# Kernel optimization log

Measured on AMD Instinct MI355X. Metric: run time of the kernel, lower is better.

Reference implementation:

```python
import jax, jax.numpy as jnp
import numpy as np

N_VERBS = 500
N_ROLES = 190
VOCAB = 2000
R = 6            # max_role_count
EMB = 512        # embed_hidden == lstm_hidden
MLP = 1024       # mlp_hidden
C = 512          # conv base size
H = W = 7
NP = H * W
NC = C + 2       # conv channels + 2 coord channels


def _lin(k, fan_in, fan_out):
    kw, kb = jax.random.split(k)
    s = 1.0 / np.sqrt(fan_in)
    return (jax.random.uniform(kw, (fan_in, fan_out), jnp.float32, -s, s),
            jax.random.uniform(kb, (fan_out,), jnp.float32, -s, s))


def setup_inputs() -> dict:
    key = jax.random.key(0)
    ks = jax.random.split(key, 16)
    inp = {}
    inp['conv_feat'] = jax.random.normal(ks[0], (2, C, H, W), jnp.float32)
    inp['verbs'] = jax.random.randint(ks[1], (2,), 0, N_VERBS, jnp.int32)
    inp['roles'] = jax.random.randint(ks[2], (2, R), 0, N_ROLES, jnp.int32)
    inp['verb_emb'] = jax.random.normal(ks[3], (N_VERBS, EMB), jnp.float32)
    inp['role_emb'] = jax.random.normal(ks[4], (N_ROLES + 1, EMB), jnp.float32)
    inp['vW1'], inp['vb1'] = _lin(ks[5], NP * C, MLP)
    inp['vW2'], inp['vb2'] = _lin(ks[6], MLP, MLP)
    inp['vW3'], inp['vb3'] = _lin(ks[7], MLP, N_VERBS)
    inp['gW1'], inp['gb1'] = _lin(ks[8], 2 * NC + EMB, MLP)
    inp['gW2'], inp['gb2'] = _lin(ks[9], MLP, MLP)
    inp['gW3'], inp['gb3'] = _lin(ks[10], MLP, 2 * MLP)
    inp['gW4'], inp['gb4'] = _lin(ks[11], 2 * MLP, 4 * MLP)
    inp['fW1'], inp['fb1'] = _lin(ks[12], 4 * MLP, 4 * MLP)
    inp['fW2'], inp['fb2'] = _lin(ks[13], 4 * MLP, 2 * MLP)
    inp['fW3'], inp['fb3'] = _lin(ks[14], 2 * MLP, VOCAB)
    return inp


def _coords():
    c = jnp.linspace(-4.0, 4.0, H)
    x = jnp.broadcast_to(c[None, :], (H, W))   # x varies along width
    y = jnp.broadcast_to(c[:, None], (H, W))   # y varies along height
    return jnp.stack([x, y]).reshape(2, NP).T  # [NP, 2]


def reference(conv_feat, verbs, roles, verb_emb, role_emb,
              vW1, vb1, vW2, vb2, vW3, vb3,
              gW1, gb1, gW2, gb2, gW3, gb3, gW4, gb4,
              fW1, fb1, fW2, fb2, fW3, fb3):
    relu = jax.nn.relu
    B = conv_feat.shape[0]

    # verb head
    flat = conv_feat.reshape(B, NP * C)
    v = relu(flat @ vW1 + vb1)
    v = relu(v @ vW2 + vb2)
    verb_pred = v @ vW3 + vb3                                  # [B, N_VERBS]

    # role-verb query
    rv = (verb_emb[verbs][:, None, :] * role_emb[roles]).reshape(B * R, EMB)

    # per-role conv features + coord channels -> [Bu, NP, NC]
    feat = jnp.broadcast_to(conv_feat[:, None], (B, R, C, H, W)).reshape(B * R, C, NP)
    feat = jnp.concatenate([feat.transpose(0, 2, 1),
                            jnp.broadcast_to(_coords()[None], (B * R, NP, 2))], axis=2)

    # first g layer: concat([o_j, o_i, qst]) @ gW1 == split matmuls + broadcast add
    Wa, Wb, Wc = gW1[:NC], gW1[NC:2 * NC], gW1[2 * NC:]
    A = feat @ Wa          # pairs with conv1 (index j)
    Bm = feat @ Wb         # pairs with conv2 (index i)
    Q = rv @ Wc
    h = relu(A[:, None, :, :] + Bm[:, :, None, :] + Q[:, None, None, :] + gb1)  # [Bu, NP, NP, MLP]
    h = relu(h @ gW2 + gb2)
    h = relu(h @ gW3 + gb3)
    h = relu(h @ gW4 + gb4)                                    # [Bu, NP, NP, 4*MLP]
    g = h.sum(axis=(1, 2))                                     # [Bu, 4*MLP]

    f = relu(g @ fW1 + fb1)
    f = relu(f @ fW2 + fb2)
    f = f @ fW3 + fb3                                          # [Bu, VOCAB]
    role_predict = f.reshape(B, R, VOCAB)
    return verb_pred, role_predict
```

## Files before the change

### kernel.cpp

```cpp
#include <hip/hip_runtime.h>
#include <cstdint>

typedef _Float16 f16;
typedef f16 f16x8 __attribute__((ext_vector_type(8)));
typedef f16 f16x4 __attribute__((ext_vector_type(4)));
typedef float f32x4 __attribute__((ext_vector_type(4)));

#define GROUP_ROWS 2560
#define VALID_ROWS 2401
#define TPG 10
#define NGROUP 12

template <bool B> struct BoolC { static constexpr bool value = B; };

__device__ __forceinline__ void gll16(const void* g, void* l) {
  __builtin_amdgcn_global_load_lds((const __attribute__((address_space(1))) void*)g,
                                   (__attribute__((address_space(3))) void*)l, 16, 0, 0);
}

__global__ void wtrans_all(const float* __restrict__ gW2, const float* __restrict__ gW3,
                           const float* __restrict__ gW4, f16* __restrict__ W2t,
                           f16* __restrict__ W3t, f16* __restrict__ W4t) {
  __shared__ float t[32][33];
  int blk = blockIdx.x;
  const float* W; f16* Wt; int K, N, local;
  if (blk < 1024)      { W = gW2; Wt = W2t; K = 1024; N = 1024; local = blk; }
  else if (blk < 3072) { W = gW3; Wt = W3t; K = 1024; N = 2048; local = blk - 1024; }
  else                 { W = gW4; Wt = W4t; K = 2048; N = 4096; local = blk - 3072; }
  int ntn = N >> 5;
  int k0 = (local / ntn) * 32, n0 = (local % ntn) * 32;
  int tx = threadIdx.x & 31, ty = threadIdx.x >> 5;
#pragma unroll
  for (int j = 0; j < 4; ++j)
    t[ty + j * 8][tx] = W[(size_t)(k0 + ty + j * 8) * N + n0 + tx];
  __syncthreads();
#pragma unroll
  for (int j = 0; j < 4; ++j)
    Wt[(size_t)(n0 + ty + j * 8) * K + k0 + tx] = (f16)t[tx][ty + j * 8];
}

__global__ void build_rv(const float* __restrict__ verb_emb, const float* __restrict__ role_emb,
                         const int* __restrict__ verbs, const int* __restrict__ roles,
                         float* __restrict__ rv) {
  int g = blockIdx.x;
  int b = g / 6;
  int v = verbs[b], ro = roles[g];
  for (int e = threadIdx.x; e < 512; e += 256)
    rv[g * 512 + e] = verb_emb[(size_t)v * 512 + e] * role_emb[(size_t)ro * 512 + e];
}

__global__ void build_AB(const float* __restrict__ conv, const float* __restrict__ gW1,
                         float* __restrict__ A, float* __restrict__ Bm) {
  int blk = blockIdx.x;
  int nq = blk & 3, bp = blk >> 2;
  int p = bp % 49, b = bp / 49;
  int n = nq * 256 + threadIdx.x;
  float accA = 0.f, accB = 0.f;
  for (int k = 0; k < 514; ++k) {
    float s;
    if (k < 512) s = conv[((size_t)b * 512 + k) * 49 + p];
    else {
      int c7 = (k == 512) ? (p % 7) : (p / 7);
      s = (float)(c7 - 3) * (4.0f / 3.0f);
    }
    accA = fmaf(s, gW1[(size_t)k * 1024 + n], accA);
    accB = fmaf(s, gW1[(size_t)(514 + k) * 1024 + n], accB);
  }
  size_t row = ((size_t)b * 49 + p) * 1024;
  A[row + n] = accA;
  Bm[row + n] = accB;
}

__global__ void build_h1(const float* __restrict__ A, const float* __restrict__ Bm,
                         const float* __restrict__ Q, const float* __restrict__ gb1,
                         f16* __restrict__ h1, int g0) {
  int rc = blockIdx.x;
  int gl = rc / GROUP_ROWS;
  int li = rc % GROUP_ROWS;
  int g = g0 + gl;
  int b = g / 6;
  int kk = threadIdx.x * 4;
  f16x4* dst = (f16x4*)(h1 + (size_t)rc * 1024 + kk);
  if (li >= VALID_ROWS) {
    f16x4 z = {(f16)0.f, (f16)0.f, (f16)0.f, (f16)0.f};
    *dst = z;
    return;
  }
  int i = li / 49, j = li % 49;
  const float4 a = *(const float4*)(A + ((size_t)b * 49 + j) * 1024 + kk);
  const float4 bb = *(const float4*)(Bm + ((size_t)b * 49 + i) * 1024 + kk);
  const float4 q = *(const float4*)(Q + (size_t)g * 1024 + kk);
  const float4 bi = *(const float4*)(gb1 + kk);
  float v0 = a.x + bb.x + q.x + bi.x;
  float v1 = a.y + bb.y + q.y + bi.y;
  float v2 = a.z + bb.z + q.z + bi.z;
  float v3 = a.w + bb.w + q.w + bi.w;
  f16x4 r;
  r.x = (f16)(v0 > 0.f ? v0 : 0.f);
  r.y = (f16)(v1 > 0.f ? v1 : 0.f);
  r.z = (f16)(v2 > 0.f ? v2 : 0.f);
  r.w = (f16)(v3 > 0.f ? v3 : 0.f);
  *dst = r;
}

#define WV4 asm volatile("s_waitcnt vmcnt(4)" ::: "memory")
#define WV0 asm volatile("s_waitcnt vmcnt(0)" ::: "memory")

#define LDSA(buf, mf, cc) (*(const f16x8*)(ldsc + (buf)*32768 + arow + (mf)*2048 + (cc)*16))
#define LDSB(buf, nf, cc) (*(const f16x8*)(ldsc + 65536 + (buf)*32768 + brow + (nf)*2048 + (cc)*16))

#define LOADB(BF, buf) { \
  BF[0][0] = LDSB(buf, 0, c0); BF[0][1] = LDSB(buf, 0, c1); \
  BF[1][0] = LDSB(buf, 1, c0); BF[1][1] = LDSB(buf, 1, c1); \
  BF[2][0] = LDSB(buf, 2, c0); BF[2][1] = LDSB(buf, 2, c1); \
  BF[3][0] = LDSB(buf, 3, c0); BF[3][1] = LDSB(buf, 3, c1); }

#define STAGE_A(t, h) { \
  const f16* _g = Aglo + (long)(h) * (128L * K) + (long)(t) * 64; \
  char* _l = ldsc + ((t)&1)*32768 + ((h)*128 + wave*16)*128; \
  gll16(_g, _l); gll16(_g + 8L*K, _l + 1024); }

#define STAGE_B(t, h) { \
  const f16* _g = Bglo + (long)(h) * (128L * K) + (long)(t) * 64; \
  char* _l = ldsc + 65536 + ((t)&1)*32768 + ((h)*128 + wave*16)*128; \
  gll16(_g, _l); gll16(_g + 8L*K, _l + 1024); }

#define PHASE(q, buf, BF, STG, WT, POST) { \
  f16x8 a00 = LDSA(buf, 2*(q), c0);   f16x8 a01 = LDSA(buf, 2*(q), c1); \
  f16x8 a10 = LDSA(buf, 2*(q)+1, c0); f16x8 a11 = LDSA(buf, 2*(q)+1, c1); \
  STG; \
  WT; \
  __builtin_amdgcn_s_barrier(); \
  __builtin_amdgcn_s_setprio(1); \
  _Pragma("unroll") \
  for (int nf = 0; nf < 4; ++nf) { \
    acc[2*(q)][nf]   = __builtin_amdgcn_mfma_f32_16x16x32_f16(a00, BF[nf][0], acc[2*(q)][nf], 0, 0, 0); \
    acc[2*(q)][nf]   = __builtin_amdgcn_mfma_f32_16x16x32_f16(a01, BF[nf][1], acc[2*(q)][nf], 0, 0, 0); \
    acc[2*(q)+1][nf] = __builtin_amdgcn_mfma_f32_16x16x32_f16(a10, BF[nf][0], acc[2*(q)+1][nf], 0, 0, 0); \
    acc[2*(q)+1][nf] = __builtin_amdgcn_mfma_f32_16x16x32_f16(a11, BF[nf][1], acc[2*(q)+1][nf], 0, 0, 0); \
  } \
  __builtin_amdgcn_s_setprio(0); \
  POST; \
  __builtin_amdgcn_s_barrier(); \
}

template <int FUSED>
__global__ __launch_bounds__(512, 2)
void gemm256(const f16* __restrict__ A, const f16* __restrict__ Bt,
             const float* __restrict__ bias, f16* __restrict__ C,
             float* __restrict__ P, int N, int K, int ntiles, int mtile_off) {
  __shared__ __align__(16) char ldsbuf[131072];
  char* ldsc = ldsbuf;
  const int tid = threadIdx.x;
  const int wave = tid >> 6, lane = tid & 63;
  const int wm = wave >> 2, wn = wave & 3;
  const int lr = lane & 15, lk = lane >> 4;
  const int c0 = lk ^ (lr & 7), c1 = c0 ^ 4;
  const int arow = (wm * 128 + lr) * 128;
  const int brow = (wn * 64 + lr) * 128;

  int nwg = gridDim.x, id = blockIdx.x;
  int qq = nwg >> 3, rr8 = nwg & 7;
  int xcd = id & 7, idx = id >> 3;
  int wg = (xcd < rr8 ? xcd * (qq + 1) : rr8 * (qq + 1) + (xcd - rr8) * qq) + idx;
  const int mtile = wg / ntiles, ntile = wg % ntiles;
  const long m0 = (long)mtile * 256, n0 = (long)ntile * 256;

  const int srow = lane >> 3;
  const int schunk = (lane & 7) ^ srow;
  const f16* Aglo = A + (m0 + wave * 16 + srow) * (long)K + schunk * 8;
  const f16* Bglo = Bt + (n0 + wave * 16 + srow) * (long)K + schunk * 8;

  f32x4 acc[8][4] = {};
  f16x8 bFa[4][2], bFb[4][2];

  const int NI = K >> 7;

  STAGE_B(0, 0); STAGE_B(0, 1);
  STAGE_A(0, 0); STAGE_A(0, 1);
  STAGE_B(1, 0); STAGE_B(1, 1);
  WV4;
  __builtin_amdgcn_s_barrier();
  LOADB(bFa, 0);

  auto run_iter = [&](int i, auto lastTag) {
    constexpr bool LAST = decltype(lastTag)::value;
    PHASE(0, 0, bFa, STAGE_A(2*i+1, 0), ;, ;);
    PHASE(1, 0, bFa, STAGE_A(2*i+1, 1), ;, ;);
    PHASE(2, 0, bFa, if constexpr (!LAST) STAGE_B(2*i+2, 0), ;, ;);
    PHASE(3, 0, bFa, if constexpr (!LAST) STAGE_B(2*i+2, 1),
                 if constexpr (LAST) { WV0; } else { WV4; },
                 LOADB(bFb, 1));
    PHASE(0, 1, bFb, if constexpr (!LAST) STAGE_A(2*i+2, 0), ;, ;);
    PHASE(1, 1, bFb, if constexpr (!LAST) STAGE_A(2*i+2, 1), ;, ;);
    PHASE(2, 1, bFb, if constexpr (!LAST) STAGE_B(2*i+3, 0), ;, ;);
    PHASE(3, 1, bFb, if constexpr (!LAST) STAGE_B(2*i+3, 1),
                 if constexpr (!LAST) { WV4; },
                 if constexpr (!LAST) LOADB(bFa, 0));
  };
#pragma unroll 1
  for (int i = 0; i < NI - 1; ++i) run_iter(i, BoolC<false>{});
  run_iter(NI - 1, BoolC<true>{});

  if (FUSED == 0) {
#pragma unroll
    for (int mf = 0; mf < 8; ++mf) {
      const long row = m0 + wm * 128 + mf * 16 + lk * 4;
#pragma unroll
      for (int nf = 0; nf < 4; ++nf) {
        const long col = n0 + wn * 64 + nf * 16 + lr;
        const float bv = bias[col];
#pragma unroll
        for (int r = 0; r < 4; ++r) {
          float v = acc[mf][nf][r] + bv;
          v = v > 0.f ? v : 0.f;
          C[(row + r) * N + col] = (f16)v;
        }
      }
    }
  } else {
    float* csum = (float*)ldsc;
    const int mrel = (mtile % TPG) * 256 + wm * 128;
#pragma unroll
    for (int nf = 0; nf < 4; ++nf) {
      const int col = (int)n0 + wn * 64 + nf * 16 + lr;
      const float bv = bias[col];
      float s = 0.f;
#pragma unroll
      for (int mf = 0; mf < 8; ++mf) {
        const int rb = mrel + mf * 16 + lk * 4;
#pragma unroll
        for (int r = 0; r < 4; ++r) {
          float v = acc[mf][nf][r] + bv;
          v = v > 0.f ? v : 0.f;
          if (rb + r < VALID_ROWS) s += v;
        }
      }
      s += __shfl_xor(s, 16);
      s += __shfl_xor(s, 32);
      if (lk == 0) csum[wm * 256 + wn * 64 + nf * 16 + lr] = s;
    }
    __syncthreads();
    for (int t = tid; t < 256; t += 512)
      P[(long)(mtile_off + mtile) * N + n0 + t] = csum[t] + csum[256 + t];
  }
}

__global__ void reduce_g(const float* __restrict__ P, float* __restrict__ g) {
  int idx = blockIdx.x * 256 + threadIdx.x;
  if (idx >= NGROUP * 4096) return;
  int gi = idx >> 12, n = idx & 4095;
  float s = 0.f;
#pragma unroll
  for (int t = 0; t < TPG; ++t) s += P[(size_t)(gi * TPG + t) * 4096 + n];
  g[idx] = s;
}

template <int M>
__global__ void skinny_part(const float* __restrict__ X, const float* __restrict__ W,
                            float* __restrict__ P, int K, int N, int kchunk) {
  int n = blockIdx.x * 256 + threadIdx.x;
  int k0 = blockIdx.y * kchunk;
  int k1 = k0 + kchunk;
  if (k1 > K) k1 = K;
  if (n >= N) return;
  float acc[M];
#pragma unroll
  for (int m = 0; m < M; ++m) acc[m] = 0.f;
  for (int k = k0; k < k1; ++k) {
    float w = W[(size_t)k * N + n];
#pragma unroll
    for (int m = 0; m < M; ++m) acc[m] = fmaf(X[(size_t)m * K + k], w, acc[m]);
  }
#pragma unroll
  for (int m = 0; m < M; ++m) P[((size_t)blockIdx.y * M + m) * N + n] = acc[m];
}

template <int RELU>
__global__ void skinny_fin(const float* __restrict__ P, const float* __restrict__ bias,
                           float* __restrict__ dst, int M, int N, int KC) {
  int idx = blockIdx.x * 256 + threadIdx.x;
  if (idx >= M * N) return;
  int m = idx / N, n = idx - m * N;
  float s = bias ? bias[n] : 0.f;
  for (int kc = 0; kc < KC; ++kc) s += P[((size_t)kc * M + m) * N + n];
  if (RELU) s = s > 0.f ? s : 0.f;
  dst[idx] = s;
}

static inline void skinny(const float* X, const float* W, const float* bias, float* dst,
                          float* sp, int Mrows, int K, int N, int relu, hipStream_t stream) {
  int KC = K >> 4;
  if (KC > 64) KC = 64;
  if (KC < 1) KC = 1;
  int kchunk = (K + KC - 1) / KC;
  dim3 g1((N + 255) / 256, KC);
  if (Mrows == 2)
    skinny_part<2><<<g1, 256, 0, stream>>>(X, W, sp, K, N, kchunk);
  else
    skinny_part<12><<<g1, 256, 0, stream>>>(X, W, sp, K, N, kchunk);
  int blocks = (Mrows * N + 255) / 256;
  if (relu)
    skinny_fin<1><<<blocks, 256, 0, stream>>>(sp, bias, dst, Mrows, N, KC);
  else
    skinny_fin<0><<<blocks, 256, 0, stream>>>(sp, bias, dst, Mrows, N, KC);
}

extern "C" void kernel_launch(void* const* d_in, const int* in_sizes, int n_in,
                              void* d_out, int out_size, void* d_ws, size_t ws_size,
                              hipStream_t stream) {
  const float* conv = (const float*)d_in[0];
  const int* verbs = (const int*)d_in[1];
  const int* roles = (const int*)d_in[2];
  const float* verb_emb = (const float*)d_in[3];
  const float* role_emb = (const float*)d_in[4];
  const float* vW1 = (const float*)d_in[5];
  const float* vb1 = (const float*)d_in[6];
  const float* vW2 = (const float*)d_in[7];
  const float* vb2 = (const float*)d_in[8];
  const float* vW3 = (const float*)d_in[9];
  const float* vb3 = (const float*)d_in[10];
  const float* gW1 = (const float*)d_in[11];
  const float* gb1 = (const float*)d_in[12];
  const float* gW2 = (const float*)d_in[13];
  const float* gb2 = (const float*)d_in[14];
  const float* gW3 = (const float*)d_in[15];
  const float* gb3 = (const float*)d_in[16];
  const float* gW4 = (const float*)d_in[17];
  const float* gb4 = (const float*)d_in[18];
  const float* fW1 = (const float*)d_in[19];
  const float* fb1 = (const float*)d_in[20];
  const float* fW2 = (const float*)d_in[21];
  const float* fb2 = (const float*)d_in[22];
  const float* fW3 = (const float*)d_in[23];
  const float* fb3 = (const float*)d_in[24];
  float* out = (float*)d_out;

  char* w = (char*)d_ws;
  auto alloc = [&](size_t bytes) {
    char* p = w;
    w += (bytes + 255) & ~(size_t)255;
    return p;
  };
  f16* W2t = (f16*)alloc((size_t)1024 * 1024 * 2);
  f16* W3t = (f16*)alloc((size_t)2048 * 1024 * 2);
  f16* W4t = (f16*)alloc((size_t)4096 * 2048 * 2);
  float* P4 = (float*)alloc((size_t)NGROUP * TPG * 4096 * 4);
  float* Abuf = (float*)alloc((size_t)2 * 49 * 1024 * 4);
  float* Bbuf = (float*)alloc((size_t)2 * 49 * 1024 * 4);
  float* Qbuf = (float*)alloc((size_t)12 * 1024 * 4);
  float* rvb = (float*)alloc((size_t)12 * 512 * 4);
  float* gbuf = (float*)alloc((size_t)12 * 4096 * 4);
  float* sp = (float*)alloc((size_t)64 * 12 * 4096 * 4);
  float* f1b = (float*)alloc((size_t)12 * 4096 * 4);
  float* f2b = (float*)alloc((size_t)12 * 2048 * 4);
  float* v1b = (float*)alloc((size_t)2 * 1024 * 4);
  float* v2b = (float*)alloc((size_t)2 * 1024 * 4);

  size_t used = (size_t)(w - (char*)d_ws);
  size_t remain = ws_size > used ? ws_size - used : 0;
  static const int opts[6] = {12, 6, 4, 3, 2, 1};
  int gpc = 1;
  for (int i = 0; i < 6; ++i) {
    size_t need = (size_t)opts[i] * GROUP_ROWS * 4096 * 2 + 4096;
    if (need <= remain) { gpc = opts[i]; break; }
  }
  f16* h1 = (f16*)alloc((size_t)gpc * GROUP_ROWS * 1024 * 2);
  f16* h2 = (f16*)alloc((size_t)gpc * GROUP_ROWS * 1024 * 2);
  f16* h3 = (f16*)alloc((size_t)gpc * GROUP_ROWS * 2048 * 2);
  int nchunks = NGROUP / gpc;

  wtrans_all<<<1024 + 2048 + 8192, 256, 0, stream>>>(gW2, gW3, gW4, W2t, W3t, W4t);

  build_rv<<<12, 256, 0, stream>>>(verb_emb, role_emb, verbs, roles, rvb);
  build_AB<<<98 * 4, 256, 0, stream>>>(conv, gW1, Abuf, Bbuf);
  skinny(rvb, gW1 + (size_t)1028 * 1024, nullptr, Qbuf, sp, 12, 512, 1024, 0, stream);

  skinny(conv, vW1, vb1, v1b, sp, 2, 25088, 1024, 1, stream);
  skinny(v1b, vW2, vb2, v2b, sp, 2, 1024, 1024, 1, stream);
  skinny(v2b, vW3, vb3, out, sp, 2, 1024, 500, 0, stream);

  for (int c = 0; c < nchunks; ++c) {
    int g0 = c * gpc;
    int Mc = gpc * GROUP_ROWS;
    int mt = Mc / 256;
    build_h1<<<Mc, 256, 0, stream>>>(Abuf, Bbuf, Qbuf, gb1, h1, g0);
    gemm256<0><<<4 * mt, 512, 0, stream>>>(h1, W2t, gb2, h2, nullptr, 1024, 1024, 4, 0);
    gemm256<0><<<8 * mt, 512, 0, stream>>>(h2, W3t, gb3, h3, nullptr, 2048, 1024, 8, 0);
    gemm256<1><<<16 * mt, 512, 0, stream>>>(h3, W4t, gb4, nullptr, P4, 4096, 2048, 16, g0 * TPG);
  }
  reduce_g<<<(NGROUP * 4096 + 255) / 256, 256, 0, stream>>>(P4, gbuf);

  skinny(gbuf, fW1, fb1, f1b, sp, 12, 4096, 4096, 1, stream);
  skinny(f1b, fW2, fb2, f2b, sp, 12, 4096, 2048, 1, stream);
  skinny(f2b, fW3, fb3, out + 1000, sp, 12, 2048, 2000, 0, stream);

  (void)in_sizes; (void)n_in; (void)out_size; (void)ws_size;
}
```

Baseline: 1.162 ms.

## Switch GEMM inner loop to 32x32x16 MFMA and stage epilogue through LDS

Replaces the 16x16x32 f16 MFMA tiling with 32x32x16 MFMA instructions, so each wave computes a 128x64 tile as 4x2 blocks of 32x32 with f32x16 accumulators. LDS fragment addressing and the XOR swizzle keys are recomputed for the new lane layout. This needs fewer LDS fragment reads and fewer MFMA issues per unit of work. The non-fused epilogue now writes bias+ReLU results into LDS and then emits coalesced 16-byte row stores, and the fused reduction is adapted to the new register layout. The cost is extra barriers and an LDS round trip in the epilogue.

Result: slower. 1.268 ms (+9.1%).

```diff
diff --git a/kernel.cpp b/kernel.cpp
--- a/kernel.cpp
+++ b/kernel.cpp
@@ -5,6 +5,7 @@
 typedef f16 f16x8 __attribute__((ext_vector_type(8)));
 typedef f16 f16x4 __attribute__((ext_vector_type(4)));
 typedef float f32x4 __attribute__((ext_vector_type(4)));
+typedef float f32x16 __attribute__((ext_vector_type(16)));
 
 #define GROUP_ROWS 2560
 #define VALID_ROWS 2401
@@ -106,14 +107,14 @@
 #define WV4 asm volatile("s_waitcnt vmcnt(4)" ::: "memory")
 #define WV0 asm volatile("s_waitcnt vmcnt(0)" ::: "memory")
 
-#define LDSA(buf, mf, cc) (*(const f16x8*)(ldsc + (buf)*32768 + arow + (mf)*2048 + (cc)*16))
-#define LDSB(buf, nf, cc) (*(const f16x8*)(ldsc + 65536 + (buf)*32768 + brow + (nf)*2048 + (cc)*16))
+#define LDSA(buf, q, CK) (*(const f16x8*)(ldsc + (buf)*32768 + arow + (q)*4096 + (CK)))
+#define LDSB(buf, nb, CK) (*(const f16x8*)(ldsc + 65536 + (buf)*32768 + brow + (nb)*4096 + (CK)))
 
 #define LOADB(BF, buf) { \
-  BF[0][0] = LDSB(buf, 0, c0); BF[0][1] = LDSB(buf, 0, c1); \
-  BF[1][0] = LDSB(buf, 1, c0); BF[1][1] = LDSB(buf, 1, c1); \
-  BF[2][0] = LDSB(buf, 2, c0); BF[2][1] = LDSB(buf, 2, c1); \
-  BF[3][0] = LDSB(buf, 3, c0); BF[3][1] = LDSB(buf, 3, c1); }
+  BF[0][0] = LDSB(buf, 0, ck0); BF[0][1] = LDSB(buf, 0, ck1); \
+  BF[0][2] = LDSB(buf, 0, ck2); BF[0][3] = LDSB(buf, 0, ck3); \
+  BF[1][0] = LDSB(buf, 1, ck0); BF[1][1] = LDSB(buf, 1, ck1); \
+  BF[1][2] = LDSB(buf, 1, ck2); BF[1][3] = LDSB(buf, 1, ck3); }
 
 #define STAGE_A(t, h) { \
   const f16* _g = Aglo + (long)(h) * (128L * K) + (long)(t) * 64; \
@@ -126,19 +127,20 @@
   gll16(_g, _l); gll16(_g + 8L*K, _l + 1024); }
 
 #define PHASE(q, buf, BF, STG, WT, POST) { \
-  f16x8 a00 = LDSA(buf, 2*(q), c0);   f16x8 a01 = LDSA(buf, 2*(q), c1); \
-  f16x8 a10 = LDSA(buf, 2*(q)+1, c0); f16x8 a11 = LDSA(buf, 2*(q)+1, c1); \
+  f16x8 a0 = LDSA(buf, q, ck0); f16x8 a1 = LDSA(buf, q, ck1); \
+  f16x8 a2 = LDSA(buf, q, ck2); f16x8 a3 = LDSA(buf, q, ck3); \
   STG; \
   WT; \
   __builtin_amdgcn_s_barrier(); \
   __builtin_amdgcn_s_setprio(1); \
-  _Pragma("unroll") \
-  for (int nf = 0; nf < 4; ++nf) { \
-    acc[2*(q)][nf]   = __builtin_amdgcn_mfma_f32_16x16x32_f16(a00, BF[nf][0], acc[2*(q)][nf], 0, 0, 0); \
-    acc[2*(q)][nf]   = __builtin_amdgcn_mfma_f32_16x16x32_f16(a01, BF[nf][1], acc[2*(q)][nf], 0, 0, 0); \
-    acc[2*(q)+1][nf] = __builtin_amdgcn_mfma_f32_16x16x32_f16(a10, BF[nf][0], acc[2*(q)+1][nf], 0, 0, 0); \
-    acc[2*(q)+1][nf] = __builtin_amdgcn_mfma_f32_16x16x32_f16(a11, BF[nf][1], acc[2*(q)+1][nf], 0, 0, 0); \
-  } \
+  acc[q][0] = __builtin_amdgcn_mfma_f32_32x32x16_f16(a0, BF[0][0], acc[q][0], 0, 0, 0); \
+  acc[q][1] = __builtin_amdgcn_mfma_f32_32x32x16_f16(a0, BF[1][0], acc[q][1], 0, 0, 0); \
+  acc[q][0] = __builtin_amdgcn_mfma_f32_32x32x16_f16(a1, BF[0][1], acc[q][0], 0, 0, 0); \
+  acc[q][1] = __builtin_amdgcn_mfma_f32_32x32x16_f16(a1, BF[1][1], acc[q][1], 0, 0, 0); \
+  acc[q][0] = __builtin_amdgcn_mfma_f32_32x32x16_f16(a2, BF[0][2], acc[q][0], 0, 0, 0); \
+  acc[q][1] = __builtin_amdgcn_mfma_f32_32x32x16_f16(a2, BF[1][2], acc[q][1], 0, 0, 0); \
+  acc[q][0] = __builtin_amdgcn_mfma_f32_32x32x16_f16(a3, BF[0][3], acc[q][0], 0, 0, 0); \
+  acc[q][1] = __builtin_amdgcn_mfma_f32_32x32x16_f16(a3, BF[1][3], acc[q][1], 0, 0, 0); \
   __builtin_amdgcn_s_setprio(0); \
   POST; \
   __builtin_amdgcn_s_barrier(); \
@@ -154,10 +156,14 @@
   const int tid = threadIdx.x;
   const int wave = tid >> 6, lane = tid & 63;
   const int wm = wave >> 2, wn = wave & 3;
-  const int lr = lane & 15, lk = lane >> 4;
-  const int c0 = lk ^ (lr & 7), c1 = c0 ^ 4;
-  const int arow = (wm * 128 + lr) * 128;
-  const int brow = (wn * 64 + lr) * 128;
+  const int l31 = lane & 31, hi = lane >> 5;
+  const int key = lane & 7;
+  const int ck0 = ((0 + hi) ^ key) * 16;
+  const int ck1 = ((2 + hi) ^ key) * 16;
+  const int ck2 = ((4 + hi) ^ key) * 16;
+  const int ck3 = ((6 + hi) ^ key) * 16;
+  const int arow = (wm * 128 + l31) * 128;
+  const int brow = (wn * 64 + l31) * 128;
 
   int nwg = gridDim.x, id = blockIdx.x;
   int qq = nwg >> 3, rr8 = nwg & 7;
@@ -171,8 +177,8 @@
   const f16* Aglo = A + (m0 + wave * 16 + srow) * (long)K + schunk * 8;
   const f16* Bglo = Bt + (n0 + wave * 16 + srow) * (long)K + schunk * 8;
 
-  f32x4 acc[8][4] = {};
-  f16x8 bFa[4][2], bFb[4][2];
+  f32x16 acc[4][2] = {};
+  f16x8 bFa[2][4], bFb[2][4];
 
   const int NI = K >> 7;
 
@@ -203,42 +209,54 @@
   run_iter(NI - 1, BoolC<true>{});
 
   if (FUSED == 0) {
-#pragma unroll
-    for (int mf = 0; mf < 8; ++mf) {
-      const long row = m0 + wm * 128 + mf * 16 + lk * 4;
-#pragma unroll
-      for (int nf = 0; nf < 4; ++nf) {
-        const long col = n0 + wn * 64 + nf * 16 + lr;
-        const float bv = bias[col];
-#pragma unroll
-        for (int r = 0; r < 4; ++r) {
-          float v = acc[mf][nf][r] + bv;
+    __syncthreads();
+    f16* lt = (f16*)ldsc;
+#pragma unroll
+    for (int q = 0; q < 4; ++q) {
+#pragma unroll
+      for (int nb = 0; nb < 2; ++nb) {
+        const int lcol = wn * 64 + nb * 32 + l31;
+        const float bv = bias[n0 + lcol];
+        const int rb = wm * 128 + q * 32 + 4 * hi;
+#pragma unroll
+        for (int reg = 0; reg < 16; ++reg) {
+          const int row = rb + (reg & 3) + 8 * (reg >> 2);
+          float v = acc[q][nb][reg] + bv;
           v = v > 0.f ? v : 0.f;
-          C[(row + r) * N + col] = (f16)v;
+          lt[row * 256 + lcol] = (f16)v;
         }
       }
     }
+    __syncthreads();
+    const int r0 = tid >> 5, ch = tid & 31;
+#pragma unroll
+    for (int p = 0; p < 16; ++p) {
+      const int row = p * 16 + r0;
+      f16x8 v = *(const f16x8*)(lt + row * 256 + ch * 8);
+      *(f16x8*)(C + (m0 + row) * N + n0 + ch * 8) = v;
+    }
   } else {
+    __syncthreads();
     float* csum = (float*)ldsc;
     const int mrel = (mtile % TPG) * 256 + wm * 128;
 #pragma unroll
-    for (int nf = 0; nf < 4; ++nf) {
-      const int col = (int)n0 + wn * 64 + nf * 16 + lr;
-      const float bv = bias[col];
+    for (int nb = 0; nb < 2; ++nb) {
+      const int lcol = wn * 64 + nb * 32 + l31;
+      const float bv = bias[n0 + lcol];
       float s = 0.f;
 #pragma unroll
-      for (int mf = 0; mf < 8; ++mf) {
-        const int rb = mrel + mf * 16 + lk * 4;
-#pragma unroll
-        for (int r = 0; r < 4; ++r) {
-          float v = acc[mf][nf][r] + bv;
+      for (int q = 0; q < 4; ++q) {
+        const int rb = mrel + q * 32 + 4 * hi;
+#pragma unroll
+        for (int reg = 0; reg < 16; ++reg) {
+          const int row = rb + (reg & 3) + 8 * (reg >> 2);
+          float v = acc[q][nb][reg] + bv;
           v = v > 0.f ? v : 0.f;
-          if (rb + r < VALID_ROWS) s += v;
+          if (row < VALID_ROWS) s += v;
         }
       }
-      s += __shfl_xor(s, 16);
       s += __shfl_xor(s, 32);
-      if (lk == 0) csum[wm * 256 + wn * 64 + nf * 16 + lr] = s;
+      if (lane < 32) csum[wm * 256 + wn * 64 + nb * 32 + lane] = s;
     }
     __syncthreads();
     for (int t = tid; t < 256; t += 512)
```
